# Kernel tuning notes

Hardware: AMD Instinct MI355X
Metric: run time of the kernel (lower is better)

Reference implementation:

```python
import jax, jax.numpy as jnp
import numpy as np

N = 50000      # nodes
E = 800000     # edges (avg in-degree 16, first N are self-loops)
H = 8          # heads
D = 16         # per-head dim (out_dim in the torch module)
IN = 128       # in_dim (= H*D)
SCALE = float(np.sqrt(D))


def setup_inputs() -> dict:
    key = jax.random.key(0)
    ks = jax.random.split(key, 8)
    query = jax.random.normal(ks[0], (N, IN), jnp.float32)
    key_x = jax.random.normal(ks[1], (N, IN), jnp.float32)
    value = jax.random.normal(ks[2], (N, IN), jnp.float32)
    # nn.Linear weights [out_features, in_features], no bias (use_bias=False)
    w_std = 1.0 / np.sqrt(IN)
    WQ = jax.random.normal(ks[3], (H * D, IN), jnp.float32) * w_std
    WK = jax.random.normal(ks[4], (H * D, IN), jnp.float32) * w_std
    WV = jax.random.normal(ks[5], (H * D, IN), jnp.float32) * w_std
    # edges: self-loops for every node (guarantees in-degree >= 1) + random edges
    loops = jnp.arange(N, dtype=jnp.int32)
    rsrc = jax.random.randint(ks[6], (E - N,), 0, N, jnp.int32)
    rdst = jax.random.randint(ks[7], (E - N,), 0, N, jnp.int32)
    edge_src = jnp.concatenate([loops, rsrc])
    edge_dst = jnp.concatenate([loops, rdst])
    return {"query": query, "key": key_x, "value": value,
            "WQ": WQ, "WK": WK, "WV": WV,
            "edge_src": edge_src, "edge_dst": edge_dst}


def reference(query, key, value, WQ, WK, WV, edge_src, edge_dst):
    n = query.shape[0]
    Qh = (query @ WQ.T).reshape(n, H, D)   # [N,H,D]
    Kh = (key @ WK.T).reshape(n, H, D)
    Vh = (value @ WV.T).reshape(n, H, D)
    # per-edge score: sum over head dim of K[src] * Q[dst]  (src_dot_dst)
    s = jnp.einsum('ehd,ehd->eh', Kh[edge_src], Qh[edge_dst])  # [E,H]
    # scaled_exp: exp(clamp(score / sqrt(D), -5, 5))
    a = jnp.exp(jnp.clip(s / SCALE, -5.0, 5.0))                # [E,H]
    # scatter-sum weighted V and normalizer z to destination nodes
    wV = jax.ops.segment_sum(a[:, :, None] * Vh[edge_src], edge_dst, num_segments=n)  # [N,H,D]
    z = jax.ops.segment_sum(a, edge_dst, num_segments=n)                               # [N,H]
    return wV / z[:, :, None]
```

## Files before the change

### kernel.cpp

```cpp
#include <hip/hip_runtime.h>

#define HD  128
#define CAP 64

typedef short bf16x8 __attribute__((ext_vector_type(8)));
typedef float f32x4  __attribute__((ext_vector_type(4)));

static __device__ __forceinline__ unsigned short f2bf_bits(float f) {
    union { float f; unsigned u; } x; x.f = f;
    unsigned r = x.u + 0x7FFF + ((x.u >> 16) & 1);
    return (unsigned short)(r >> 16);
}
static __device__ __forceinline__ float bf2f(unsigned short s) {
    union { unsigned u; float f; } x; x.u = ((unsigned)s) << 16;
    return x.f;
}

__global__ __launch_bounds__(256) void k_pre(
    const float* __restrict__ wq, const float* __restrict__ wk,
    const float* __restrict__ wv, short* __restrict__ wb,
    int* __restrict__ cursor, int n)
{
    int t = blockIdx.x * blockDim.x + threadIdx.x;
    int nthr = gridDim.x * blockDim.x;
    for (int i = t; i < 3 * 16384 / 4; i += nthr) {
        int flat = i * 4;
        int m = flat >> 14;
        int off = flat & 16383;
        const float* W = (m == 0) ? wq : (m == 1) ? wk : wv;
        float4 v = *(const float4*)(W + off);
        short4 s;
        s.x = (short)f2bf_bits(v.x);
        s.y = (short)f2bf_bits(v.y);
        s.z = (short)f2bf_bits(v.z);
        s.w = (short)f2bf_bits(v.w);
        *(short4*)(wb + flat) = s;
    }
    for (int i = t; i < n; i += nthr) cursor[i] = 0;
}

__global__ __launch_bounds__(256) void k_scat(
    const int* __restrict__ esrc, const int* __restrict__ edst,
    int* __restrict__ cursor, int* __restrict__ csr, int E)
{
    int i = blockIdx.x * 256 + threadIdx.x;
    if (i < E) {
        int d = edst[i];
        int p = atomicAdd(&cursor[d], 1);
        if (p < CAP) csr[d * CAP + p] = esrc[i];
    }
}

__global__ __launch_bounds__(256) void k_proj(
    const float* __restrict__ q, const float* __restrict__ k, const float* __restrict__ v,
    const short* __restrict__ wb,
    float* __restrict__ qh, short* __restrict__ kvb,
    int n, int ntiles)
{
    __shared__ short wlds[16384];
    int bid = blockIdx.x;
    int m = bid % 3;
    int t0 = bid / 3;
    const float* X = (m == 0) ? q : (m == 1) ? k : v;
    const short* W = wb + m * 16384;

    int tid = threadIdx.x;
    for (int i = tid; i < 2048; i += 256) {
        int row = i >> 4, g = i & 15;
        *(bf16x8*)&wlds[row * 128 + ((g ^ (row & 15)) * 8)] =
            *(const bf16x8*)&W[row * 128 + g * 8];
    }
    __syncthreads();

    int wave = tid >> 6, lane = tid & 63;
    int lm = lane & 15, lg = lane >> 4;

    for (int tile = t0; tile < ntiles; tile += 256) {
        int row0 = tile * 64 + wave * 16;
        int arow = row0 + lm; if (arow >= n) arow = n - 1;
        const float* xp = X + (size_t)arow * HD + lg * 8;

        float4 p0[4], p1[4];
        #pragma unroll
        for (int kk = 0; kk < 4; kk++) {
            p0[kk] = *(const float4*)(xp + kk * 32);
            p1[kk] = *(const float4*)(xp + kk * 32 + 4);
        }
        bf16x8 a[4];
        #pragma unroll
        for (int kk = 0; kk < 4; kk++) {
            bf16x8 t;
            t[0] = (short)f2bf_bits(p0[kk].x); t[1] = (short)f2bf_bits(p0[kk].y);
            t[2] = (short)f2bf_bits(p0[kk].z); t[3] = (short)f2bf_bits(p0[kk].w);
            t[4] = (short)f2bf_bits(p1[kk].x); t[5] = (short)f2bf_bits(p1[kk].y);
            t[6] = (short)f2bf_bits(p1[kk].z); t[7] = (short)f2bf_bits(p1[kk].w);
            a[kk] = t;
        }

        f32x4 acc[8];
        #pragma unroll
        for (int nt = 0; nt < 8; nt++) { f32x4 z = {0.f, 0.f, 0.f, 0.f}; acc[nt] = z; }

        #pragma unroll
        for (int nt = 0; nt < 8; nt++) {
            #pragma unroll
            for (int kk = 0; kk < 4; kk++) {
                bf16x8 b = *(const bf16x8*)&wlds[(nt * 16 + lm) * 128 +
                                                 (((lg + 4 * kk) ^ lm) * 8)];
                acc[nt] = __builtin_amdgcn_mfma_f32_16x16x32_bf16(a[kk], b, acc[nt], 0, 0, 0);
            }
        }

        if (m == 0) {
            #pragma unroll
            for (int nt = 0; nt < 8; nt++)
                #pragma unroll
                for (int i = 0; i < 4; i++) {
                    int r = row0 + lg * 4 + i;
                    if (r < n) qh[(size_t)r * HD + nt * 16 + lm] = acc[nt][i];
                }
        } else {
            short* base = kvb + ((m == 1) ? 0 : HD);
            #pragma unroll
            for (int nt = 0; nt < 8; nt++)
                #pragma unroll
                for (int i = 0; i < 4; i++) {
                    int r = row0 + lg * 4 + i;
                    if (r < n) base[(size_t)r * 256 + nt * 16 + lm] =
                        (short)f2bf_bits(acc[nt][i]);
                }
        }
    }
}

__global__ __launch_bounds__(256) void k_gather(
    const float* __restrict__ qh, const short* __restrict__ kvb,
    const int* __restrict__ cursor, const int* __restrict__ csr,
    float* __restrict__ out, int n)
{
    int wave = threadIdx.x >> 6;
    int lane = threadIdx.x & 63;
    int v = blockIdx.x * 4 + wave;
    if (v >= n) return;
    int j = lane & 31;

    float4 qv = *(const float4*)&qh[(size_t)v * HD + 4 * j];
    int beg = v * CAP;
    int cnt = cursor[v]; if (cnt > CAP) cnt = CAP;
    int end = beg + cnt;

    float4 acc = {0.f, 0.f, 0.f, 0.f};
    float z = 0.f;

    int e = beg;
    for (; e + 3 < end; e += 4) {
        int u0 = csr[e];
        int u1 = csr[e + 1];
        int u2 = csr[e + 2];
        int u3 = csr[e + 3];
        ushort4 kv0 = *(const ushort4*)&kvb[(size_t)u0 * 256 + 4 * lane];
        ushort4 kv1 = *(const ushort4*)&kvb[(size_t)u1 * 256 + 4 * lane];
        ushort4 kv2 = *(const ushort4*)&kvb[(size_t)u2 * 256 + 4 * lane];
        ushort4 kv3 = *(const ushort4*)&kvb[(size_t)u3 * 256 + 4 * lane];
        float x00 = bf2f(kv0.x), x01 = bf2f(kv0.y), x02 = bf2f(kv0.z), x03 = bf2f(kv0.w);
        float x10 = bf2f(kv1.x), x11 = bf2f(kv1.y), x12 = bf2f(kv1.z), x13 = bf2f(kv1.w);
        float x20 = bf2f(kv2.x), x21 = bf2f(kv2.y), x22 = bf2f(kv2.z), x23 = bf2f(kv2.w);
        float x30 = bf2f(kv3.x), x31 = bf2f(kv3.y), x32 = bf2f(kv3.z), x33 = bf2f(kv3.w);
        float p0 = x00 * qv.x + x01 * qv.y + x02 * qv.z + x03 * qv.w;
        float p1 = x10 * qv.x + x11 * qv.y + x12 * qv.z + x13 * qv.w;
        float p2 = x20 * qv.x + x21 * qv.y + x22 * qv.z + x23 * qv.w;
        float p3 = x30 * qv.x + x31 * qv.y + x32 * qv.z + x33 * qv.w;
        p0 += __shfl_xor(p0, 1); p1 += __shfl_xor(p1, 1);
        p2 += __shfl_xor(p2, 1); p3 += __shfl_xor(p3, 1);
        p0 += __shfl_xor(p0, 2); p1 += __shfl_xor(p1, 2);
        p2 += __shfl_xor(p2, 2); p3 += __shfl_xor(p3, 2);
        float a0 = __expf(fminf(fmaxf(p0 * 0.25f, -5.f), 5.f));
        float a1 = __expf(fminf(fmaxf(p1 * 0.25f, -5.f), 5.f));
        float a2 = __expf(fminf(fmaxf(p2 * 0.25f, -5.f), 5.f));
        float a3 = __expf(fminf(fmaxf(p3 * 0.25f, -5.f), 5.f));
        float av0 = __shfl_xor(a0, 32);
        float av1 = __shfl_xor(a1, 32);
        float av2 = __shfl_xor(a2, 32);
        float av3 = __shfl_xor(a3, 32);
        z += (a0 + a1) + (a2 + a3);
        acc.x += av0 * x00 + av1 * x10 + av2 * x20 + av3 * x30;
        acc.y += av0 * x01 + av1 * x11 + av2 * x21 + av3 * x31;
        acc.z += av0 * x02 + av1 * x12 + av2 * x22 + av3 * x32;
        acc.w += av0 * x03 + av1 * x13 + av2 * x23 + av3 * x33;
    }
    for (; e < end; ++e) {
        int u = csr[e];
        ushort4 kv = *(const ushort4*)&kvb[(size_t)u * 256 + 4 * lane];
        float x0 = bf2f(kv.x), x1 = bf2f(kv.y), x2 = bf2f(kv.z), x3 = bf2f(kv.w);
        float p = x0 * qv.x + x1 * qv.y + x2 * qv.z + x3 * qv.w;
        p += __shfl_xor(p, 1);
        p += __shfl_xor(p, 2);
        float a = __expf(fminf(fmaxf(p * 0.25f, -5.f), 5.f));
        float av = __shfl_xor(a, 32);
        z += a;
        acc.x += av * x0; acc.y += av * x1; acc.z += av * x2; acc.w += av * x3;
    }

    float zz = __shfl_xor(z, 32);
    if (lane >= 32) {
        float inv = 1.f / zz;
        float4 o = { acc.x * inv, acc.y * inv, acc.z * inv, acc.w * inv };
        *(float4*)&out[(size_t)v * HD + 4 * j] = o;
    }
}

extern "C" void kernel_launch(void* const* d_in, const int* in_sizes, int n_in,
                              void* d_out, int out_size, void* d_ws, size_t ws_size,
                              hipStream_t stream)
{
    const float* query = (const float*)d_in[0];
    const float* key   = (const float*)d_in[1];
    const float* value = (const float*)d_in[2];
    const float* WQ    = (const float*)d_in[3];
    const float* WK    = (const float*)d_in[4];
    const float* WV    = (const float*)d_in[5];
    const int*   esrc  = (const int*)d_in[6];
    const int*   edst  = (const int*)d_in[7];
    int n = in_sizes[0] / HD;
    int E = in_sizes[6];

    char* ws = (char*)d_ws;
    size_t off = 0;
    auto carve = [&](size_t bytes) -> void* {
        void* p = ws + off;
        off += (bytes + 255) & ~size_t(255);
        return p;
    };
    float* qh     = (float*)carve((size_t)n * HD * 4);
    short* kvb    = (short*)carve((size_t)n * 256 * 2);
    short* wb     = (short*)carve((size_t)3 * 16384 * 2);
    int*   cursor = (int*)carve((size_t)n * 4);
    int*   csr    = (int*)carve((size_t)n * CAP * 4);
    (void)ws_size;

    k_pre<<<64, 256, 0, stream>>>(WQ, WK, WV, wb, cursor, n);

    k_scat<<<(E + 255) / 256, 256, 0, stream>>>(esrc, edst, cursor, csr, E);

    int ntiles = (n + 63) / 64;
    k_proj<<<768, 256, 0, stream>>>(query, key, value, wb, qh, kvb, n, ntiles);

    k_gather<<<(n + 3) / 4, 256, 0, stream>>>(qh, kvb, cursor, csr,
                                              (float*)d_out, n);
}
```

Baseline: 140.1 us.

## Process two edges per wave half with 16-byte loads in gather kernel

Rearranges the gather wave so each half-wave (32 lanes) processes a different edge, with each lane loading 8 bf16 values (16 bytes) instead of 4. Each edge's K/V row is handled by 16 K-lanes and 16 V-lanes, which shortens the dot-product shuffle reduction. The partial accumulators of the two halves are combined at the end, and the tail is handled by predication instead of a scalar remainder loop. The exp/clamp is rewritten as exp2 with med3 clamping. The goal is more bytes per load instruction and fewer shuffles and exp calls per edge, at the cost of more registers and a final cross-half reduction.

```diff
diff --git a/kernel.cpp b/kernel.cpp
--- a/kernel.cpp
+++ b/kernel.cpp
@@ -5,6 +5,7 @@
 
 typedef short bf16x8 __attribute__((ext_vector_type(8)));
 typedef float f32x4  __attribute__((ext_vector_type(4)));
+typedef unsigned short us8 __attribute__((ext_vector_type(8)));
 
 static __device__ __forceinline__ unsigned short f2bf_bits(float f) {
     union { float f; unsigned u; } x; x.f = f;
@@ -138,74 +139,78 @@
     const int* __restrict__ cursor, const int* __restrict__ csr,
     float* __restrict__ out, int n)
 {
+    const float C  = 0.36067376022224085f;
+    const float CL = 7.213475204444817f;
+
     int wave = threadIdx.x >> 6;
     int lane = threadIdx.x & 63;
     int v = blockIdx.x * 4 + wave;
     if (v >= n) return;
-    int j = lane & 31;
-
-    float4 qv = *(const float4*)&qh[(size_t)v * HD + 4 * j];
+    int sub  = lane & 15;
+    int quad = lane >> 4;
+    int kv_off = (quad & 1) * 128 + sub * 8;
+
+    float4 qa = *(const float4*)&qh[(size_t)v * HD + sub * 8];
+    float4 qb = *(const float4*)&qh[(size_t)v * HD + sub * 8 + 4];
+
     int beg = v * CAP;
     int cnt = cursor[v]; if (cnt > CAP) cnt = CAP;
     int end = beg + cnt;
 
-    float4 acc = {0.f, 0.f, 0.f, 0.f};
+    float acc[8];
+    #pragma unroll
+    for (int i = 0; i < 8; i++) acc[i] = 0.f;
     float z = 0.f;
 
-    int e = beg;
-    for (; e + 3 < end; e += 4) {
-        int u0 = csr[e];
-        int u1 = csr[e + 1];
-        int u2 = csr[e + 2];
-        int u3 = csr[e + 3];
-        ushort4 kv0 = *(const ushort4*)&kvb[(size_t)u0 * 256 + 4 * lane];
-        ushort4 kv1 = *(const ushort4*)&kvb[(size_t)u1 * 256 + 4 * lane];
-        ushort4 kv2 = *(const ushort4*)&kvb[(size_t)u2 * 256 + 4 * lane];
-        ushort4 kv3 = *(const ushort4*)&kvb[(size_t)u3 * 256 + 4 * lane];
-        float x00 = bf2f(kv0.x), x01 = bf2f(kv0.y), x02 = bf2f(kv0.z), x03 = bf2f(kv0.w);
-        float x10 = bf2f(kv1.x), x11 = bf2f(kv1.y), x12 = bf2f(kv1.z), x13 = bf2f(kv1.w);
-        float x20 = bf2f(kv2.x), x21 = bf2f(kv2.y), x22 = bf2f(kv2.z), x23 = bf2f(kv2.w);
-        float x30 = bf2f(kv3.x), x31 = bf2f(kv3.y), x32 = bf2f(kv3.z), x33 = bf2f(kv3.w);
-        float p0 = x00 * qv.x + x01 * qv.y + x02 * qv.z + x03 * qv.w;
-        float p1 = x10 * qv.x + x11 * qv.y + x12 * qv.z + x13 * qv.w;
-        float p2 = x20 * qv.x + x21 * qv.y + x22 * qv.z + x23 * qv.w;
-        float p3 = x30 * qv.x + x31 * qv.y + x32 * qv.z + x33 * qv.w;
-        p0 += __shfl_xor(p0, 1); p1 += __shfl_xor(p1, 1);
-        p2 += __shfl_xor(p2, 1); p3 += __shfl_xor(p3, 1);
-        p0 += __shfl_xor(p0, 2); p1 += __shfl_xor(p1, 2);
-        p2 += __shfl_xor(p2, 2); p3 += __shfl_xor(p3, 2);
-        float a0 = __expf(fminf(fmaxf(p0 * 0.25f, -5.f), 5.f));
-        float a1 = __expf(fminf(fmaxf(p1 * 0.25f, -5.f), 5.f));
-        float a2 = __expf(fminf(fmaxf(p2 * 0.25f, -5.f), 5.f));
-        float a3 = __expf(fminf(fmaxf(p3 * 0.25f, -5.f), 5.f));
-        float av0 = __shfl_xor(a0, 32);
-        float av1 = __shfl_xor(a1, 32);
-        float av2 = __shfl_xor(a2, 32);
-        float av3 = __shfl_xor(a3, 32);
-        z += (a0 + a1) + (a2 + a3);
-        acc.x += av0 * x00 + av1 * x10 + av2 * x20 + av3 * x30;
-        acc.y += av0 * x01 + av1 * x11 + av2 * x21 + av3 * x31;
-        acc.z += av0 * x02 + av1 * x12 + av2 * x22 + av3 * x32;
-        acc.w += av0 * x03 + av1 * x13 + av2 * x23 + av3 * x33;
-    }
-    for (; e < end; ++e) {
-        int u = csr[e];
-        ushort4 kv = *(const ushort4*)&kvb[(size_t)u * 256 + 4 * lane];
-        float x0 = bf2f(kv.x), x1 = bf2f(kv.y), x2 = bf2f(kv.z), x3 = bf2f(kv.w);
-        float p = x0 * qv.x + x1 * qv.y + x2 * qv.z + x3 * qv.w;
-        p += __shfl_xor(p, 1);
-        p += __shfl_xor(p, 2);
-        float a = __expf(fminf(fmaxf(p * 0.25f, -5.f), 5.f));
-        float av = __shfl_xor(a, 32);
-        z += a;
-        acc.x += av * x0; acc.y += av * x1; acc.z += av * x2; acc.w += av * x3;
-    }
-
-    float zz = __shfl_xor(z, 32);
-    if (lane >= 32) {
+    for (int e = beg; e < end; e += 4) {
+        bool vA1 = (e + 1 < end);
+        bool vB0 = (e + 2 < end);
+        bool vB1 = (e + 3 < end);
+        int uA0 = csr[e];
+        int uA1 = vA1 ? csr[e + 1] : uA0;
+        int uB0 = vB0 ? csr[e + 2] : uA0;
+        int uB1 = vB1 ? csr[e + 3] : uA0;
+        int uA = (quad < 2) ? uA0 : uA1;
+        int uB = (quad < 2) ? uB0 : uB1;
+        us8 hA = *(const us8*)&kvb[(size_t)uA * 256 + kv_off];
+        us8 hB = *(const us8*)&kvb[(size_t)uB * 256 + kv_off];
+
+        float yA[8], yB[8];
+        #pragma unroll
+        for (int i = 0; i < 8; i++) { yA[i] = bf2f(hA[i]); yB[i] = bf2f(hB[i]); }
+
+        float pA = yA[0]*qa.x + yA[1]*qa.y + yA[2]*qa.z + yA[3]*qa.w
+                 + yA[4]*qb.x + yA[5]*qb.y + yA[6]*qb.z + yA[7]*qb.w;
+        float pB = yB[0]*qa.x + yB[1]*qa.y + yB[2]*qa.z + yB[3]*qa.w
+                 + yB[4]*qb.x + yB[5]*qb.y + yB[6]*qb.z + yB[7]*qb.w;
+        pA += __shfl_xor(pA, 1);
+        pB += __shfl_xor(pB, 1);
+
+        float aA = exp2f(__builtin_amdgcn_fmed3f(pA * C, -CL, CL));
+        float aB = exp2f(__builtin_amdgcn_fmed3f(pB * C, -CL, CL));
+        aA = (quad < 2 || vA1) ? aA : 0.f;
+        aB = ((quad < 2) ? vB0 : vB1) ? aB : 0.f;
+
+        z += aA + aB;
+
+        float avA = __shfl_xor(aA, 16);
+        float avB = __shfl_xor(aB, 16);
+        #pragma unroll
+        for (int i = 0; i < 8; i++)
+            acc[i] += avA * yA[i] + avB * yB[i];
+    }
+
+    float zt = z + __shfl_xor(z, 32);
+    #pragma unroll
+    for (int i = 0; i < 8; i++) acc[i] += __shfl_xor(acc[i], 32);
+    float zz = __shfl_xor(zt, 16);
+
+    if (quad == 1) {
         float inv = 1.f / zz;
-        float4 o = { acc.x * inv, acc.y * inv, acc.z * inv, acc.w * inv };
-        *(float4*)&out[(size_t)v * HD + 4 * j] = o;
+        float4 o0 = { acc[0]*inv, acc[1]*inv, acc[2]*inv, acc[3]*inv };
+        float4 o1 = { acc[4]*inv, acc[5]*inv, acc[6]*inv, acc[7]*inv };
+        *(float4*)&out[(size_t)v * HD + sub * 8]     = o0;
+        *(float4*)&out[(size_t)v * HD + sub * 8 + 4] = o1;
     }
 }
 
```

Measured after the change: 148.5 us. 1.06x slower.
